# Performance work log

Hardware: AMD Instinct MI355X
Metric: run time of the kernel (lower is better)

## Reference

```python
import jax, jax.numpy as jnp
import numpy as np

HIDDEN = 1024
N_HEADS = 16
N_KV_HEADS = 4
HEAD_DIM = HIDDEN // N_HEADS  # 64
GROUPS = N_HEADS // N_KV_HEADS  # 4


def setup_inputs() -> dict:
    key = jax.random.key(0)
    k1, k2, k3, k4 = jax.random.split(key, 4)
    B, T = 2, 2048
    s = 0.02
    x = jax.random.normal(k1, (B, T, HIDDEN), dtype=jnp.float32)
    Wq = jax.random.normal(k2, (HIDDEN, N_HEADS * HEAD_DIM), dtype=jnp.float32) * s
    Wkv = jax.random.normal(k3, (HIDDEN, 2 * N_KV_HEADS * HEAD_DIM), dtype=jnp.float32) * s
    Wo = jax.random.normal(k4, (N_HEADS * HEAD_DIM, HIDDEN), dtype=jnp.float32) * s
    return {"x": x, "Wq": Wq, "Wkv": Wkv, "Wo": Wo}


def reference(x, Wq, Wkv, Wo):
    B, T, _ = x.shape
    scale = HEAD_DIM ** -0.5
    q = (x @ Wq).reshape(B, T, N_HEADS, HEAD_DIM).transpose(0, 2, 1, 3)  # [B,H,T,D]
    kv = x @ Wkv
    k, v = jnp.split(kv, 2, axis=-1)
    k = k.reshape(B, T, N_KV_HEADS, HEAD_DIM).transpose(0, 2, 1, 3)  # [B,Hkv,T,D]
    v = v.reshape(B, T, N_KV_HEADS, HEAD_DIM).transpose(0, 2, 1, 3)
    # repeat_interleave over head dim -> [B,H,T,D]
    k = jnp.repeat(k, GROUPS, axis=1)
    v = jnp.repeat(v, GROUPS, axis=1)
    scores = jnp.einsum("bhqd,bhkd->bhqk", q, k) * scale
    causal = jnp.triu(jnp.ones((T, T), dtype=bool), k=1)
    scores = jnp.where(causal[None, None], -jnp.inf, scores)
    w = jax.nn.softmax(scores, axis=-1)
    out = jnp.einsum("bhqk,bhkd->bhqd", w, v)
    out = out.transpose(0, 2, 1, 3).reshape(B, T, N_HEADS * HEAD_DIM)
    return out @ Wo
```

## Files before the change

### kernel.cpp

```cpp
#include <hip/hip_runtime.h>

using bf16x8 = __attribute__((ext_vector_type(8))) __bf16;
using f32x4  = __attribute__((ext_vector_type(4))) float;

__device__ __forceinline__ short f2bf(float f) {
  unsigned u = __builtin_bit_cast(unsigned, f);
  u += 0x7fffu + ((u >> 16) & 1u);
  return (short)(u >> 16);
}

__device__ __forceinline__ void gll16(const void* g, void* l) {
  __builtin_amdgcn_global_load_lds((const __attribute__((address_space(1))) unsigned*)g,
                                   (__attribute__((address_space(3))) unsigned*)l, 16, 0, 0);
}

__global__ __launch_bounds__(256) void fused_pre(const float* __restrict__ x,
                                                 const float* __restrict__ Wq,
                                                 const float* __restrict__ Wkv,
                                                 const float* __restrict__ Wo,
                                                 short* __restrict__ xb,
                                                 short* __restrict__ Wqkvt,
                                                 short* __restrict__ Wot) {
  const int bx = blockIdx.x, tid = threadIdx.x;
  if (bx < 4096) {
    int i = (bx * 256 + tid) * 4;
    float4 f = *(const float4*)(&x[i]);
    short4 o;
    o.x = f2bf(f.x); o.y = f2bf(f.y); o.z = f2bf(f.z); o.w = f2bf(f.w);
    *(short4*)(&xb[i]) = o;
    return;
  }
  __shared__ short tile[32][33];
  const float* src; short* dst; int C, ti;
  if (bx < 5120)      { src = Wq;  dst = Wqkvt;               C = 1024; ti = bx - 4096; }
  else if (bx < 5632) { src = Wkv; dst = Wqkvt + 1024 * 1024; C = 512;  ti = bx - 5120; }
  else                { src = Wo;  dst = Wot;                 C = 1024; ti = bx - 5632; }
  int ctiles = C >> 5;
  int c0 = (ti % ctiles) * 32, r0 = (ti / ctiles) * 32;
  int tx = tid & 31, ty = tid >> 5;
  for (int i = ty; i < 32; i += 8)
    tile[i][tx] = f2bf(src[(r0 + i) * C + c0 + tx]);
  __syncthreads();
  for (int i = ty; i < 32; i += 8)
    dst[(c0 + i) * 1024L + r0 + tx] = tile[tx][i];
}

template <bool OUT_BF16, bool WRITE_VT>
__global__ __launch_bounds__(256) void gemm_bt(const short* __restrict__ A,
                                               const short* __restrict__ Bt,
                                               void* __restrict__ Cout,
                                               short* __restrict__ Vt,
                                               int N, int K) {
  __shared__ __attribute__((aligned(16))) short sA[2][64 * 64];
  __shared__ __attribute__((aligned(16))) short sB[2][128 * 64];
  const int tid  = threadIdx.x;
  const int bm   = blockIdx.y * 64, bn = blockIdx.x * 128;
  const int wave = tid >> 6, lane = tid & 63;
  const int wm = (wave >> 1) * 32, wn = (wave & 1) * 64;
  const int qd = lane >> 4, c16 = lane & 15;

  f32x4 acc[2][4] = {};

  auto stage = [&](int it, int d) {
    int k0 = it * 64;
#pragma unroll
    for (int i = 0; i < 2; i++) {
      int c = i * 256 + tid;
      int r = c >> 3, cc = c & 7;
      gll16(&A[(bm + r) * (long)K + k0 + ((cc ^ (r & 7)) * 8)],
            &sA[d][(i * 256 + wave * 64) * 8]);
    }
#pragma unroll
    for (int i = 0; i < 4; i++) {
      int c = i * 256 + tid;
      int r = c >> 3, cc = c & 7;
      gll16(&Bt[(bn + r) * (long)K + k0 + ((cc ^ (r & 7)) * 8)],
            &sB[d][(i * 256 + wave * 64) * 8]);
    }
  };

  const int niter = K >> 6;
  stage(0, 0);
  for (int it = 0; it < niter; it++) {
    const int cur = it & 1;
    asm volatile("" ::: "memory");
    __builtin_amdgcn_s_barrier();
    if (it + 1 < niter) {
      stage(it + 1, cur ^ 1);
      asm volatile("s_waitcnt vmcnt(6)" ::: "memory");
    } else {
      asm volatile("s_waitcnt vmcnt(0)" ::: "memory");
    }
    __builtin_amdgcn_s_barrier();
    asm volatile("" ::: "memory");

    bf16x8 af[2][2], bfr[4][2];
#pragma unroll
    for (int mt = 0; mt < 2; mt++) {
      int rr = wm + mt * 16 + c16;
#pragma unroll
      for (int ks = 0; ks < 2; ks++)
        af[mt][ks] = *(const bf16x8*)(&sA[cur][rr * 64 + (((ks * 4 + qd) ^ (rr & 7)) * 8)]);
    }
#pragma unroll
    for (int nt = 0; nt < 4; nt++) {
      int rr = wn + nt * 16 + c16;
#pragma unroll
      for (int ks = 0; ks < 2; ks++)
        bfr[nt][ks] = *(const bf16x8*)(&sB[cur][rr * 64 + (((ks * 4 + qd) ^ (rr & 7)) * 8)]);
    }
#pragma unroll
    for (int ks = 0; ks < 2; ks++)
#pragma unroll
      for (int mt = 0; mt < 2; mt++)
#pragma unroll
        for (int nt = 0; nt < 4; nt++)
          acc[mt][nt] = __builtin_amdgcn_mfma_f32_16x16x32_bf16(af[mt][ks], bfr[nt][ks],
                                                                acc[mt][nt], 0, 0, 0);
  }

#pragma unroll
  for (int mt = 0; mt < 2; mt++)
#pragma unroll
    for (int nt = 0; nt < 4; nt++) {
      long row0 = bm + wm + mt * 16 + qd * 4;
      long col  = bn + wn + nt * 16 + c16;
      short4 p;
#pragma unroll
      for (int r = 0; r < 4; r++) {
        float v = acc[mt][nt][r];
        if constexpr (OUT_BF16) ((short*)Cout)[(row0 + r) * N + col] = f2bf(v);
        else                    ((float*)Cout)[(row0 + r) * N + col] = v;
        if constexpr (WRITE_VT)
          ((short*)&p)[r] = f2bf(v);
      }
      if constexpr (WRITE_VT) {
        if (col >= 1280) {
          int d = (int)col - 1280;
          int b = (int)(row0 >> 11), t = (int)(row0 & 2047);
          *(short4*)(&Vt[((long)(b * 256 + d)) * 2048 + t]) = p;
        }
      }
    }
}

#define CSOFT 0.18033688f
#define CMAX  (CSOFT * 12.0f)

__global__ __launch_bounds__(256, 4) void attn_kernel(const short* __restrict__ QKV,
                                                      const short* __restrict__ Vt,
                                                      short* __restrict__ Aout) {
  const int bx = blockIdx.x;
  const int qt = (bx < 512) ? (127 - (bx >> 3)) : ((bx >> 3) - 64);
  const int kvh = (bx >> 1) & 3, b = bx & 1;
  const int bkv = b * 4 + kvh;
  const int tid = threadIdx.x;
  const int w = tid >> 6, lane = tid & 63;
  const int qd = lane >> 4, c16 = lane & 15;
  const int h = kvh * 4 + w;
  const int q0 = qt * 16;

  __shared__ __attribute__((aligned(16))) short sK[2][64 * 64];
  __shared__ __attribute__((aligned(16))) short sVt[64 * 64];
  __shared__ __attribute__((aligned(16))) short sP[4][16 * 72];

  auto stageK = [&](int kt, int d) {
#pragma unroll
    for (int i = 0; i < 2; i++) {
      int c = i * 256 + tid;
      int r = c >> 3, cc = c & 7;
      gll16(&QKV[((long)(b * 2048 + kt * 64 + r)) * 1536 + 1024 + kvh * 64 + ((cc ^ (r & 7)) * 8)],
            &sK[d][(i * 256 + w * 64) * 8]);
    }
  };
  auto stageV = [&](int kt) {
#pragma unroll
    for (int i = 0; i < 2; i++) {
      int c = i * 256 + tid;
      int r = c >> 3, cc = c & 7;
      gll16(&Vt[((long)(bkv * 64 + r)) * 2048 + kt * 64 + ((cc ^ (r & 7)) * 8)],
            &sVt[(i * 256 + w * 64) * 8]);
    }
  };

  stageK(0, 0);

  bf16x8 qf[2];
  {
    long tok = (long)b * 2048 + q0 + c16;
#pragma unroll
    for (int ks = 0; ks < 2; ks++)
      qf[ks] = *(const bf16x8*)(&QKV[tok * 1536 + h * 64 + ks * 32 + qd * 8]);
  }

  f32x4 Ot[4] = {};
  float l_i = 0.f;

  const int ntiles = (qt >> 2) + 1;
  for (int kt = 0; kt < ntiles; kt++) {
    const int cur = kt & 1;
    asm volatile("" ::: "memory");
    __builtin_amdgcn_s_barrier();
    stageV(kt);
    if (kt + 1 < ntiles) {
      stageK(kt + 1, cur ^ 1);
      asm volatile("s_waitcnt vmcnt(4)" ::: "memory");
    } else {
      asm volatile("s_waitcnt vmcnt(2)" ::: "memory");
    }
    __builtin_amdgcn_s_barrier();
    asm volatile("" ::: "memory");

    f32x4 St[4];
#pragma unroll
    for (int jc = 0; jc < 4; jc++) {
      int rr = jc * 16 + c16;
      bf16x8 kf0 = *(const bf16x8*)(&sK[cur][rr * 64 + ((0 + qd) ^ (rr & 7)) * 8]);
      bf16x8 kf1 = *(const bf16x8*)(&sK[cur][rr * 64 + ((4 + qd) ^ (rr & 7)) * 8]);
      f32x4 z = {};
      z = __builtin_amdgcn_mfma_f32_16x16x32_bf16(kf0, qf[0], z, 0, 0, 0);
      z = __builtin_amdgcn_mfma_f32_16x16x32_bf16(kf1, qf[1], z, 0, 0, 0);
      St[jc] = z;
    }

    if (kt == ntiles - 1) {
      int qg = q0 + c16 - kt * 64;
#pragma unroll
      for (int jc = 0; jc < 4; jc++)
#pragma unroll
        for (int r = 0; r < 4; r++)
          if (jc * 16 + qd * 4 + r > qg) St[jc][r] = -3e38f;
    }

    {
      float rs = 0.f;
#pragma unroll
      for (int jc = 0; jc < 4; jc++) {
        unsigned u[4];
#pragma unroll
        for (int r = 0; r < 4; r++) {
          float p = exp2f(fmaf(CSOFT, St[jc][r], -CMAX));
          u[r] = __builtin_bit_cast(unsigned, p) & 0xffff0000u;
          rs += __builtin_bit_cast(float, u[r]);
        }
        int2 pk;
        pk.x = (int)((u[0] >> 16) | u[1]);
        pk.y = (int)((u[2] >> 16) | u[3]);
        *(int2*)(&sP[w][c16 * 72 + jc * 16 + qd * 4]) = pk;
      }
      l_i += rs;
    }
    asm volatile("s_waitcnt lgkmcnt(0)" ::: "memory");

    if (kt + 1 < ntiles) asm volatile("s_waitcnt vmcnt(2)" ::: "memory");
    else                 asm volatile("s_waitcnt vmcnt(0)" ::: "memory");
    __builtin_amdgcn_s_barrier();
    asm volatile("" ::: "memory");

#pragma unroll
    for (int ks2 = 0; ks2 < 2; ks2++) {
      bf16x8 pf = *(const bf16x8*)(&sP[w][c16 * 72 + ks2 * 32 + qd * 8]);
#pragma unroll
      for (int dt = 0; dt < 4; dt++) {
        int rr = dt * 16 + c16;
        bf16x8 vf = *(const bf16x8*)(&sVt[rr * 64 + (((ks2 * 4 + qd) ^ (rr & 7)) * 8)]);
        Ot[dt] = __builtin_amdgcn_mfma_f32_16x16x32_bf16(vf, pf, Ot[dt], 0, 0, 0);
      }
    }
  }

  {
    float l = l_i;
    l += __shfl_xor(l, 16, 64);
    l += __shfl_xor(l, 32, 64);
    float inv = 1.f / l;
    long tok = (long)b * 2048 + q0 + c16;
#pragma unroll
    for (int dt = 0; dt < 4; dt++) {
      short4 o;
      o.x = f2bf(Ot[dt][0] * inv);
      o.y = f2bf(Ot[dt][1] * inv);
      o.z = f2bf(Ot[dt][2] * inv);
      o.w = f2bf(Ot[dt][3] * inv);
      *(short4*)(&Aout[tok * 1024 + h * 64 + dt * 16 + qd * 4]) = o;
    }
  }
}

extern "C" void kernel_launch(void* const* d_in, const int* in_sizes, int n_in,
                              void* d_out, int out_size, void* d_ws, size_t ws_size,
                              hipStream_t stream) {
  const float* x   = (const float*)d_in[0];
  const float* Wq  = (const float*)d_in[1];
  const float* Wkv = (const float*)d_in[2];
  const float* Wo  = (const float*)d_in[3];

  char* ws = (char*)d_ws;
  short* xb    = (short*)(ws);
  short* Wqkvt = (short*)(ws + 8388608);
  short* Wot   = (short*)(ws + 11534336);
  short* QKV   = (short*)(ws + 13631488);
  short* attn  = (short*)(ws + 26214400);
  short* Vtb   = (short*)d_out;

  fused_pre<<<dim3(6656), 256, 0, stream>>>(x, Wq, Wkv, Wo, xb, Wqkvt, Wot);

  gemm_bt<true, true><<<dim3(12, 64), 256, 0, stream>>>(xb, Wqkvt, QKV, Vtb, 1536, 1024);

  attn_kernel<<<dim3(1024), 256, 0, stream>>>(QKV, Vtb, attn);

  gemm_bt<false, false><<<dim3(8, 64), 256, 0, stream>>>(attn, Wot, d_out, nullptr, 1024, 1024);
}
```

Baseline: 157.4 us.

## Enlarge GEMM tiles to 128x128 with K=32 stages and reorder attention tile schedule

The GEMM kernel now uses 128x128 output tiles per block with a K step of 32, so each wave computes a 64x64 sub-tile and reuses every LDS fragment over four MFMAs. This raises arithmetic intensity and halves the grid for both projections. The XOR swizzle on LDS rows is dropped, so 64-byte row strides may cause bank conflicts, and the smaller grid (384 and 256 blocks) may leave CUs underused. The attention block-to-query-tile mapping is also reordered into four rounds that alternate heavy and light causal tiles for better load balance.

New measurement: 172.2 us. 1.09x slower.

```diff
diff --git a/kernel.cpp b/kernel.cpp
--- a/kernel.cpp
+++ b/kernel.cpp
@@ -51,35 +51,33 @@
                                                void* __restrict__ Cout,
                                                short* __restrict__ Vt,
                                                int N, int K) {
-  __shared__ __attribute__((aligned(16))) short sA[2][64 * 64];
-  __shared__ __attribute__((aligned(16))) short sB[2][128 * 64];
+  __shared__ __attribute__((aligned(16))) short sA[2][128 * 32];
+  __shared__ __attribute__((aligned(16))) short sB[2][128 * 32];
   const int tid  = threadIdx.x;
-  const int bm   = blockIdx.y * 64, bn = blockIdx.x * 128;
+  const int bm   = blockIdx.y * 128, bn = blockIdx.x * 128;
   const int wave = tid >> 6, lane = tid & 63;
-  const int wm = (wave >> 1) * 32, wn = (wave & 1) * 64;
+  const int wm = (wave >> 1) * 64, wn = (wave & 1) * 64;
   const int qd = lane >> 4, c16 = lane & 15;
 
-  f32x4 acc[2][4] = {};
+  f32x4 acc[4][4] = {};
 
   auto stage = [&](int it, int d) {
-    int k0 = it * 64;
+    int k0 = it * 32;
 #pragma unroll
     for (int i = 0; i < 2; i++) {
       int c = i * 256 + tid;
-      int r = c >> 3, cc = c & 7;
-      gll16(&A[(bm + r) * (long)K + k0 + ((cc ^ (r & 7)) * 8)],
-            &sA[d][(i * 256 + wave * 64) * 8]);
-    }
-#pragma unroll
-    for (int i = 0; i < 4; i++) {
+      int r = c >> 2, o = c & 3;
+      gll16(&A[(bm + r) * (long)K + k0 + o * 8], &sA[d][(i * 256 + wave * 64) * 8]);
+    }
+#pragma unroll
+    for (int i = 0; i < 2; i++) {
       int c = i * 256 + tid;
-      int r = c >> 3, cc = c & 7;
-      gll16(&Bt[(bn + r) * (long)K + k0 + ((cc ^ (r & 7)) * 8)],
-            &sB[d][(i * 256 + wave * 64) * 8]);
+      int r = c >> 2, o = c & 3;
+      gll16(&Bt[(bn + r) * (long)K + k0 + o * 8], &sB[d][(i * 256 + wave * 64) * 8]);
     }
   };
 
-  const int niter = K >> 6;
+  const int niter = K >> 5;
   stage(0, 0);
   for (int it = 0; it < niter; it++) {
     const int cur = it & 1;
@@ -87,40 +85,28 @@
     __builtin_amdgcn_s_barrier();
     if (it + 1 < niter) {
       stage(it + 1, cur ^ 1);
-      asm volatile("s_waitcnt vmcnt(6)" ::: "memory");
+      asm volatile("s_waitcnt vmcnt(4)" ::: "memory");
     } else {
       asm volatile("s_waitcnt vmcnt(0)" ::: "memory");
     }
     __builtin_amdgcn_s_barrier();
     asm volatile("" ::: "memory");
 
-    bf16x8 af[2][2], bfr[4][2];
-#pragma unroll
-    for (int mt = 0; mt < 2; mt++) {
-      int rr = wm + mt * 16 + c16;
-#pragma unroll
-      for (int ks = 0; ks < 2; ks++)
-        af[mt][ks] = *(const bf16x8*)(&sA[cur][rr * 64 + (((ks * 4 + qd) ^ (rr & 7)) * 8)]);
-    }
-#pragma unroll
-    for (int nt = 0; nt < 4; nt++) {
-      int rr = wn + nt * 16 + c16;
-#pragma unroll
-      for (int ks = 0; ks < 2; ks++)
-        bfr[nt][ks] = *(const bf16x8*)(&sB[cur][rr * 64 + (((ks * 4 + qd) ^ (rr & 7)) * 8)]);
-    }
-#pragma unroll
-    for (int ks = 0; ks < 2; ks++)
-#pragma unroll
-      for (int mt = 0; mt < 2; mt++)
-#pragma unroll
-        for (int nt = 0; nt < 4; nt++)
-          acc[mt][nt] = __builtin_amdgcn_mfma_f32_16x16x32_bf16(af[mt][ks], bfr[nt][ks],
-                                                                acc[mt][nt], 0, 0, 0);
-  }
-
-#pragma unroll
-  for (int mt = 0; mt < 2; mt++)
+    bf16x8 af[4], bfr[4];
+#pragma unroll
+    for (int t = 0; t < 4; t++) {
+      af[t]  = *(const bf16x8*)(&sA[cur][(wm + t * 16 + c16) * 32 + qd * 8]);
+      bfr[t] = *(const bf16x8*)(&sB[cur][(wn + t * 16 + c16) * 32 + qd * 8]);
+    }
+#pragma unroll
+    for (int mt = 0; mt < 4; mt++)
+#pragma unroll
+      for (int nt = 0; nt < 4; nt++)
+        acc[mt][nt] = __builtin_amdgcn_mfma_f32_16x16x32_bf16(af[mt], bfr[nt], acc[mt][nt], 0, 0, 0);
+  }
+
+#pragma unroll
+  for (int mt = 0; mt < 4; mt++)
 #pragma unroll
     for (int nt = 0; nt < 4; nt++) {
       long row0 = bm + wm + mt * 16 + qd * 4;
@@ -151,8 +137,14 @@
                                                       const short* __restrict__ Vt,
                                                       short* __restrict__ Aout) {
   const int bx = blockIdx.x;
-  const int qt = (bx < 512) ? (127 - (bx >> 3)) : ((bx >> 3) - 64);
-  const int kvh = (bx >> 1) & 3, b = bx & 1;
+  const int rnd = bx >> 8, u = bx & 255, a = u >> 3;
+  int qt_;
+  if      (rnd == 0) qt_ = 127 - a;
+  else if (rnd == 1) qt_ = 64 + a;
+  else if (rnd == 2) qt_ = 63 - a;
+  else               qt_ = a;
+  const int qt = qt_;
+  const int kvh = (u >> 1) & 3, b = u & 1;
   const int bkv = b * 4 + kvh;
   const int tid = threadIdx.x;
   const int w = tid >> 6, lane = tid & 63;
@@ -236,16 +228,16 @@
       float rs = 0.f;
 #pragma unroll
       for (int jc = 0; jc < 4; jc++) {
-        unsigned u[4];
+        unsigned u4[4];
 #pragma unroll
         for (int r = 0; r < 4; r++) {
           float p = exp2f(fmaf(CSOFT, St[jc][r], -CMAX));
-          u[r] = __builtin_bit_cast(unsigned, p) & 0xffff0000u;
-          rs += __builtin_bit_cast(float, u[r]);
+          u4[r] = __builtin_bit_cast(unsigned, p) & 0xffff0000u;
+          rs += __builtin_bit_cast(float, u4[r]);
         }
         int2 pk;
-        pk.x = (int)((u[0] >> 16) | u[1]);
-        pk.y = (int)((u[2] >> 16) | u[3]);
+        pk.x = (int)((u4[0] >> 16) | u4[1]);
+        pk.y = (int)((u4[2] >> 16) | u4[3]);
         *(int2*)(&sP[w][c16 * 72 + jc * 16 + qd * 4]) = pk;
       }
       l_i += rs;
@@ -305,9 +297,9 @@
 
   fused_pre<<<dim3(6656), 256, 0, stream>>>(x, Wq, Wkv, Wo, xb, Wqkvt, Wot);
 
-  gemm_bt<true, true><<<dim3(12, 64), 256, 0, stream>>>(xb, Wqkvt, QKV, Vtb, 1536, 1024);
+  gemm_bt<true, true><<<dim3(12, 32), 256, 0, stream>>>(xb, Wqkvt, QKV, Vtb, 1536, 1024);
 
   attn_kernel<<<dim3(1024), 256, 0, stream>>>(QKV, Vtb, attn);
 
-  gemm_bt<false, false><<<dim3(8, 64), 256, 0, stream>>>(attn, Wot, d_out, nullptr, 1024, 1024);
-}
+  gemm_bt<false, false><<<dim3(8, 32), 256, 0, stream>>>(attn, Wot, d_out, nullptr, 1024, 1024);
+}
```
